# Kernel optimization log

Measured on AMD Instinct MI355X. Metric: run time of the kernel, lower is better.

## Reference

```python
import jax, jax.numpy as jnp
import numpy as np

KSIZE = 11  # kernel_size


def setup_inputs() -> dict:
    key = jax.random.key(0)
    k1, k2, k3, k4 = jax.random.split(key, 4)
    B, C, H, W, K = 4, 3, 512, 512, KSIZE
    return {
        "input1": jax.random.normal(k1, (B, C, H + K - 1, W + K - 1), jnp.float32),  # padded image
        "input2": jax.random.normal(k2, (B, K, H, W), jnp.float32),  # vertical per-pixel kernels
        "input3": jax.random.normal(k3, (B, K, H, W), jnp.float32),  # horizontal per-pixel kernels
        "input4": jax.random.normal(k4, (B, 2, H, W), jnp.float32),  # flow: ch0 = dx, ch1 = dy
    }


def _sdc_forward(input1, input2, input3, input4):
    # out[b,c,y,x] = sum_{fy,fx} bilinear(input1)[b,c, y+dy+fy, x+dx+fx] * v[b,fy,y,x] * h[b,fx,y,x]
    B, C, Hp, Wp = input1.shape
    _, K, H, W = input2.shape
    dt = input1.dtype
    dx = input4[:, 0]  # [B,H,W]
    dy = input4[:, 1]
    py = jnp.arange(H, dtype=dt)[None, :, None] + dy  # float sample base rows [B,H,W]
    px = jnp.arange(W, dtype=dt)[None, None, :] + dx
    fy0 = jnp.floor(py)
    fx0 = jnp.floor(px)
    wy = (py - fy0)[:, None]  # bilinear fractional weights [B,1,H,W]
    wx = (px - fx0)[:, None]
    iy0 = fy0.astype(jnp.int32)
    ix0 = fx0.astype(jnp.int32)

    # Since filter offsets are integers, the bilinear weights are shared across taps.
    # Fold them into extended (K+1)-tap separable kernels: one gather per (gy,gx).
    zpad = jnp.zeros((B, 1, H, W), dt)
    Vy = jnp.concatenate([input2, zpad], 1) * (1 - wy) + jnp.concatenate([zpad, input2], 1) * wy  # [B,K+1,H,W]
    Hx = jnp.concatenate([input3, zpad], 1) * (1 - wx) + jnp.concatenate([zpad, input3], 1) * wx  # [B,K+1,H,W]

    def gather(iy, ix):
        # iy, ix: [B,H,W] int -> [B,C,H,W], zero outside image bounds
        valid = (iy >= 0) & (iy < Hp) & (ix >= 0) & (ix < Wp)
        iyc = jnp.clip(iy, 0, Hp - 1)
        ixc = jnp.clip(ix, 0, Wp - 1)
        vals = jax.vmap(lambda im, y, x: im[:, y, x])(input1, iyc, ixc)  # [B,C,H,W]
        return vals * valid[:, None].astype(dt)

    out = jnp.zeros((B, C, H, W), dt)
    for gy in range(K + 1):
        for gx in range(K + 1):
            w = (Vy[:, gy] * Hx[:, gx])[:, None]  # [B,1,H,W]
            out = out + w * gather(iy0 + gy, ix0 + gx)
    return out


def reference(input1, input2, input3, input4):
    return _sdc_forward(input1, input2, input3, input4)
```

## Files before the change

kernel.cpp:

```cpp
#include <hip/hip_runtime.h>
#include <stdint.h>


typedef _Float16 half_t;
typedef half_t half2_t __attribute__((ext_vector_type(2)));

constexpr int B  = 4;
constexpr int C  = 3;
constexpr int H  = 512;
constexpr int W  = 512;
constexpr int K  = 11;
constexpr int KP = K + 1;
constexpr int Hp = H + K - 1;
constexpr int Wp = W + K - 1;
constexpr int HW = H * W;
constexpr int PLANE1 = Hp * Wp;

constexpr int TW   = 32;
constexpr int TH   = 8;
constexpr int ROWS = 32;
constexpr int COLS = 64;
constexpr int ROWB = 136;
constexpr int CHB  = ROWS * ROWB;

__global__ __launch_bounds__(256) void sdc_kernel(
    const float* __restrict__ in1,
    const float* __restrict__ in2,
    const float* __restrict__ in3,
    const float* __restrict__ in4,
    float* __restrict__ out)
{
    __shared__ char lds[C * CHB];
    __shared__ int  red[16];

    const int tid  = threadIdx.x;
    const int lane = tid & 63;
    const int wid  = tid >> 6;
    const int w = blockIdx.x * TW + (tid & (TW - 1));
    const int h = blockIdx.y * TH + (tid >> 5);
    const int b = blockIdx.z;
    const int pix = h * W + w;

    const float dx = in4[(b * 2 + 0) * HW + pix];
    const float dy = in4[(b * 2 + 1) * HW + pix];

    const float py  = (float)h + dy;
    const float px  = (float)w + dx;
    const float fy0 = floorf(py);
    const float fx0 = floorf(px);
    const float wy  = py - fy0;
    const float wx  = px - fx0;
    const int   iy0 = (int)fy0;
    const int   ix0 = (int)fx0;

    int mniy = iy0, mxiy = iy0, mnix = ix0, mxix = ix0;
    #pragma unroll
    for (int m = 1; m < 64; m <<= 1) {
        mniy = min(mniy, __shfl_xor(mniy, m, 64));
        mxiy = max(mxiy, __shfl_xor(mxiy, m, 64));
        mnix = min(mnix, __shfl_xor(mnix, m, 64));
        mxix = max(mxix, __shfl_xor(mxix, m, 64));
    }
    const int wv_mniy = mniy, wv_mxiy = mxiy;
    if (lane == 0) {
        red[wid * 4 + 0] = mniy;
        red[wid * 4 + 1] = mxiy;
        red[wid * 4 + 2] = mnix;
        red[wid * 4 + 3] = mxix;
    }
    __syncthreads();
    const int row0 = min(min(red[0], red[4]), min(red[8], red[12]));
    const int rmax = max(max(red[1], red[5]), max(red[9], red[13]));
    const int col0 = min(min(red[2], red[6]), min(red[10], red[14]));
    const int cmax = max(max(red[3], red[7]), max(red[11], red[15]));
    const bool fits = (rmax - row0 + KP <= ROWS) && (cmax - col0 + KP <= COLS);

    if (fits) {
        const float* bb1 = in1 + (size_t)b * C * PLANE1;
        #pragma unroll
        for (int it = 0; it < 12; ++it) {
            int idx = it * 256 + tid;
            int cp  = idx & 31;
            int cr  = idx >> 5;
            int c   = cr >> 5;
            int r   = cr & 31;
            int srcr = min(max(row0 + r, 0), Hp - 1);
            int gc0  = col0 + 2 * cp;
            int s0c  = min(max(gc0, 0), Wp - 1);
            int s1c  = min(max(gc0 + 1, 0), Wp - 1);
            const float* p = bb1 + (size_t)c * PLANE1 + (size_t)srcr * Wp;
            half2_t hv;
            hv.x = (half_t)p[s0c];
            hv.y = (half_t)p[s1c];
            *(uint32_t*)(lds + c * CHB + r * ROWB + cp * 4) =
                __builtin_bit_cast(uint32_t, hv);
        }
        if (tid < 192) {
            int cr = tid >> 1;
            int c  = cr >> 5;
            int r  = cr & 31;
            int cp = 32 + (tid & 1);
            int srcr = min(max(row0 + r, 0), Hp - 1);
            int gc0  = col0 + 2 * cp;
            int s0c  = min(max(gc0, 0), Wp - 1);
            int s1c  = min(max(gc0 + 1, 0), Wp - 1);
            const float* p = bb1 + (size_t)c * PLANE1 + (size_t)srcr * Wp;
            half2_t hv;
            hv.x = (half_t)p[s0c];
            hv.y = (half_t)p[s1c];
            *(uint32_t*)(lds + c * CHB + r * ROWB + cp * 4) =
                __builtin_bit_cast(uint32_t, hv);
        }
    }

    float Vye[KP], Hxe[KP];
    {
        const float* p2 = in2 + b * K * HW + pix;
        const float* p3 = in3 + b * K * HW + pix;
        float v2[K], v3[K];
        #pragma unroll
        for (int k = 0; k < K; ++k) {
            v2[k] = p2[k * HW];
            v3[k] = p3[k * HW];
        }
        const float omwy = 1.f - wy;
        const float omwx = 1.f - wx;
        #pragma unroll
        for (int g = 0; g < KP; ++g) {
            float a2 = (g < K) ? v2[g] : 0.f;
            float b2 = (g > 0) ? v2[g - 1] : 0.f;
            float vy = a2 * omwy + b2 * wy;
            int   iy = iy0 + g;
            Vye[g] = (iy >= 0 && iy < Hp) ? vy : 0.f;
            float a3 = (g < K) ? v3[g] : 0.f;
            float b3 = (g > 0) ? v3[g - 1] : 0.f;
            float hx = a3 * omwx + b3 * wx;
            int   ix = ix0 + g;
            Hxe[g] = (ix >= 0 && ix < Wp) ? hx : 0.f;
        }
    }

    float acc0 = 0.f, acc1 = 0.f, acc2 = 0.f;

    if (fits) {
        const int s  = ix0 - col0;
        const int a4 = s & ~3;
        const int e2 = s & 3;
        half2_t W2[8];
        {
            const bool is1 = (e2 == 1), is2 = (e2 == 2), is3 = (e2 == 3);
            float Wf[16];
            #pragma unroll
            for (int j = 0; j < 16; ++j) {
                float v0  = (j < 12) ? Hxe[j] : 0.f;
                float v1  = (j >= 1 && j <= 12) ? Hxe[j - 1] : 0.f;
                float v2_ = (j >= 2 && j <= 13) ? Hxe[j - 2] : 0.f;
                float v3_ = (j >= 3 && j <= 14) ? Hxe[j - 3] : 0.f;
                Wf[j] = is3 ? v3_ : (is2 ? v2_ : (is1 ? v1 : v0));
            }
            #pragma unroll
            for (int p = 0; p < 8; ++p) {
                half2_t hw;
                hw.x = (half_t)Wf[2 * p];
                hw.y = (half_t)Wf[2 * p + 1];
                W2[p] = hw;
            }
        }

        float F[ROWS];
        #pragma unroll
        for (int i = 0; i < ROWS; ++i) F[i] = (i < KP) ? Vye[i] : 0.f;
        const int sh = iy0 - row0;
        #pragma unroll
        for (int st = 16; st >= 1; st >>= 1) {
            const bool c = (sh & st) != 0;
            #pragma unroll
            for (int i = ROWS - 1; i >= 0; --i) {
                float shifted = (i - st >= 0) ? F[i - st] : 0.f;
                F[i] = c ? shifted : F[i];
            }
        }

        const int rlo = __builtin_amdgcn_readfirstlane(max(0, wv_mniy - row0));
        const int rhi = __builtin_amdgcn_readfirstlane(min(ROWS, wv_mxiy - row0 + KP));

        __syncthreads();

        const char* lb = lds + (a4 << 1);
        #pragma unroll
        for (int r = 0; r < ROWS; ++r) {
            if (r >= rlo && r < rhi) {
                float sc0 = 0.f, sc1 = 0.f, sc2 = 0.f;
                #pragma unroll
                for (int blk = 0; blk < 4; ++blk) {
                    uint2 q0 = *(const uint2*)(lb + 0 * CHB + r * ROWB + 8 * blk);
                    uint2 q1 = *(const uint2*)(lb + 1 * CHB + r * ROWB + 8 * blk);
                    uint2 q2 = *(const uint2*)(lb + 2 * CHB + r * ROWB + 8 * blk);
                    sc0 = __builtin_amdgcn_fdot2(__builtin_bit_cast(half2_t, q0.x), W2[2 * blk],     sc0, false);
                    sc0 = __builtin_amdgcn_fdot2(__builtin_bit_cast(half2_t, q0.y), W2[2 * blk + 1], sc0, false);
                    sc1 = __builtin_amdgcn_fdot2(__builtin_bit_cast(half2_t, q1.x), W2[2 * blk],     sc1, false);
                    sc1 = __builtin_amdgcn_fdot2(__builtin_bit_cast(half2_t, q1.y), W2[2 * blk + 1], sc1, false);
                    sc2 = __builtin_amdgcn_fdot2(__builtin_bit_cast(half2_t, q2.x), W2[2 * blk],     sc2, false);
                    sc2 = __builtin_amdgcn_fdot2(__builtin_bit_cast(half2_t, q2.y), W2[2 * blk + 1], sc2, false);
                }
                acc0 += F[r] * sc0;
                acc1 += F[r] * sc1;
                acc2 += F[r] * sc2;
            }
        }
    } else {
        const float* base1 = in1 + (size_t)b * C * PLANE1;
        #pragma unroll 1
        for (int gy = 0; gy < KP; ++gy) {
            const int iyc = min(max(iy0 + gy, 0), Hp - 1);
            const float* r = base1 + iyc * Wp;
            float s0 = 0.f, s1 = 0.f, s2 = 0.f;
            #pragma unroll
            for (int gx = 0; gx < KP; ++gx) {
                const int ixc = min(max(ix0 + gx, 0), Wp - 1);
                const float hx = Hxe[gx];
                s0 += hx * r[ixc];
                s1 += hx * r[PLANE1 + ixc];
                s2 += hx * r[2 * PLANE1 + ixc];
            }
            acc0 += Vye[gy] * s0;
            acc1 += Vye[gy] * s1;
            acc2 += Vye[gy] * s2;
        }
    }

    float* po = out + b * C * HW + pix;
    po[0]      = acc0;
    po[HW]     = acc1;
    po[2 * HW] = acc2;
}

extern "C" void kernel_launch(void* const* d_in, const int* in_sizes, int n_in,
                              void* d_out, int out_size, void* d_ws, size_t ws_size,
                              hipStream_t stream) {
    const float* in1 = (const float*)d_in[0];
    const float* in2 = (const float*)d_in[1];
    const float* in3 = (const float*)d_in[2];
    const float* in4 = (const float*)d_in[3];
    float* out = (float*)d_out;

    dim3 grid(W / TW, H / TH, B);
    dim3 block(TW * TH);
    sdc_kernel<<<grid, block, 0, stream>>>(in1, in2, in3, in4, out);
}
```

Measured before the change: 56.25 us.

## Shrink LDS tile rows and use wave-relative vertical window to cut registers

```diff
diff --git a/kernel.cpp b/kernel.cpp
--- a/kernel.cpp
+++ b/kernel.cpp
@@ -16,12 +16,13 @@
 constexpr int HW = H * W;
 constexpr int PLANE1 = Hp * Wp;
 
-constexpr int TW   = 32;
-constexpr int TH   = 8;
-constexpr int ROWS = 32;
-constexpr int COLS = 64;
-constexpr int ROWB = 136;
-constexpr int CHB  = ROWS * ROWB;
+constexpr int TW    = 32;
+constexpr int TH    = 8;
+constexpr int ROWS  = 28;
+constexpr int PAIRS = 34;
+constexpr int ROWB  = PAIRS * 4;
+constexpr int CHB   = ROWS * ROWB;
+constexpr int WSPAN = 24;
 
 __global__ __launch_bounds__(256) void sdc_kernel(
     const float* __restrict__ in1,
@@ -61,7 +62,8 @@
         mnix = min(mnix, __shfl_xor(mnix, m, 64));
         mxix = max(mxix, __shfl_xor(mxix, m, 64));
     }
-    const int wv_mniy = mniy, wv_mxiy = mxiy;
+    const int wv_mniy = __builtin_amdgcn_readfirstlane(mniy);
+    const int wv_mxiy = __builtin_amdgcn_readfirstlane(mxiy);
     if (lane == 0) {
         red[wid * 4 + 0] = mniy;
         red[wid * 4 + 1] = mxiy;
@@ -73,17 +75,18 @@
     const int rmax = max(max(red[1], red[5]), max(red[9], red[13]));
     const int col0 = min(min(red[2], red[6]), min(red[10], red[14]));
     const int cmax = max(max(red[3], red[7]), max(red[11], red[15]));
-    const bool fits = (rmax - row0 + KP <= ROWS) && (cmax - col0 + KP <= COLS);
+    const bool fits = (rmax - row0 + KP <= ROWS) && (cmax - col0 + KP <= 64);
 
     if (fits) {
         const float* bb1 = in1 + (size_t)b * C * PLANE1;
         #pragma unroll
-        for (int it = 0; it < 12; ++it) {
+        for (int it = 0; it < 11; ++it) {
             int idx = it * 256 + tid;
+            if (it == 10 && idx >= 2688) break;
             int cp  = idx & 31;
             int cr  = idx >> 5;
-            int c   = cr >> 5;
-            int r   = cr & 31;
+            int c   = cr / ROWS;
+            int r   = cr - c * ROWS;
             int srcr = min(max(row0 + r, 0), Hp - 1);
             int gc0  = col0 + 2 * cp;
             int s0c  = min(max(gc0, 0), Wp - 1);
@@ -95,10 +98,10 @@
             *(uint32_t*)(lds + c * CHB + r * ROWB + cp * 4) =
                 __builtin_bit_cast(uint32_t, hv);
         }
-        if (tid < 192) {
+        if (tid < 168) {
             int cr = tid >> 1;
-            int c  = cr >> 5;
-            int r  = cr & 31;
+            int c  = cr / ROWS;
+            int r  = cr - c * ROWS;
             int cp = 32 + (tid & 1);
             int srcr = min(max(row0 + r, 0), Hp - 1);
             int gc0  = col0 + 2 * cp;
@@ -140,9 +143,13 @@
         }
     }
 
+    const int rlo  = wv_mniy - row0;
+    const int jcnt = (wv_mxiy - wv_mniy) + KP;
+    const bool wave_ok = (jcnt <= WSPAN);
+
     float acc0 = 0.f, acc1 = 0.f, acc2 = 0.f;
 
-    if (fits) {
+    if (fits && wave_ok) {
         const int s  = ix0 - col0;
         const int a4 = s & ~3;
         const int e2 = s & 3;
@@ -167,35 +174,32 @@
             }
         }
 
-        float F[ROWS];
-        #pragma unroll
-        for (int i = 0; i < ROWS; ++i) F[i] = (i < KP) ? Vye[i] : 0.f;
-        const int sh = iy0 - row0;
-        #pragma unroll
-        for (int st = 16; st >= 1; st >>= 1) {
-            const bool c = (sh & st) != 0;
-            #pragma unroll
-            for (int i = ROWS - 1; i >= 0; --i) {
+        float F[WSPAN];
+        #pragma unroll
+        for (int i = 0; i < WSPAN; ++i) F[i] = (i < KP) ? Vye[i] : 0.f;
+        const int shp = iy0 - wv_mniy;
+        #pragma unroll
+        for (int st = 8; st >= 1; st >>= 1) {
+            const bool c = (shp & st) != 0;
+            #pragma unroll
+            for (int i = WSPAN - 1; i >= 0; --i) {
                 float shifted = (i - st >= 0) ? F[i - st] : 0.f;
                 F[i] = c ? shifted : F[i];
             }
         }
 
-        const int rlo = __builtin_amdgcn_readfirstlane(max(0, wv_mniy - row0));
-        const int rhi = __builtin_amdgcn_readfirstlane(min(ROWS, wv_mxiy - row0 + KP));
-
         __syncthreads();
 
-        const char* lb = lds + (a4 << 1);
-        #pragma unroll
-        for (int r = 0; r < ROWS; ++r) {
-            if (r >= rlo && r < rhi) {
+        const char* lb = lds + rlo * ROWB + (a4 << 1);
+        #pragma unroll
+        for (int j = 0; j < WSPAN; ++j) {
+            if (j < jcnt) {
                 float sc0 = 0.f, sc1 = 0.f, sc2 = 0.f;
                 #pragma unroll
                 for (int blk = 0; blk < 4; ++blk) {
-                    uint2 q0 = *(const uint2*)(lb + 0 * CHB + r * ROWB + 8 * blk);
-                    uint2 q1 = *(const uint2*)(lb + 1 * CHB + r * ROWB + 8 * blk);
-                    uint2 q2 = *(const uint2*)(lb + 2 * CHB + r * ROWB + 8 * blk);
+                    uint2 q0 = *(const uint2*)(lb + 0 * CHB + j * ROWB + 8 * blk);
+                    uint2 q1 = *(const uint2*)(lb + 1 * CHB + j * ROWB + 8 * blk);
+                    uint2 q2 = *(const uint2*)(lb + 2 * CHB + j * ROWB + 8 * blk);
                     sc0 = __builtin_amdgcn_fdot2(__builtin_bit_cast(half2_t, q0.x), W2[2 * blk],     sc0, false);
                     sc0 = __builtin_amdgcn_fdot2(__builtin_bit_cast(half2_t, q0.y), W2[2 * blk + 1], sc0, false);
                     sc1 = __builtin_amdgcn_fdot2(__builtin_bit_cast(half2_t, q1.x), W2[2 * blk],     sc1, false);
@@ -203,12 +207,13 @@
                     sc2 = __builtin_amdgcn_fdot2(__builtin_bit_cast(half2_t, q2.x), W2[2 * blk],     sc2, false);
                     sc2 = __builtin_amdgcn_fdot2(__builtin_bit_cast(half2_t, q2.y), W2[2 * blk + 1], sc2, false);
                 }
-                acc0 += F[r] * sc0;
-                acc1 += F[r] * sc1;
-                acc2 += F[r] * sc2;
+                acc0 += F[j] * sc0;
+                acc1 += F[j] * sc1;
+                acc2 += F[j] * sc2;
             }
         }
     } else {
+        if (fits) __syncthreads();
         const float* base1 = in1 + (size_t)b * C * PLANE1;
         #pragma unroll 1
         for (int gy = 0; gy < KP; ++gy) {
```

Result: no change. 55.53 us (-1.3%).
